# Optimization experiments

Hardware: AMD Instinct MI355X
Metric: run time of the kernel (lower is better)

## Reference

```python
import jax, jax.numpy as jnp
import numpy as np
import math

B, S, HID = 16, 512, 768
NUM_LABELS = 9
NUM_HEADS = 4
HEAD_DIM = HID // NUM_HEADS
MAX_REL = 5
B_PERSON = 1
I_PERSON = 2
LN_EPS = 1e-5


def setup_inputs() -> dict:
    key = jax.random.key(0)
    ks = jax.random.split(key, 16)
    w = lambda k, shp: jax.random.normal(k, shp, dtype=jnp.float32) * 0.02
    return {
        "sequence_output": jax.random.normal(ks[0], (B, S, HID), dtype=jnp.float32),
        "Wq": w(ks[1], (HID, HID)), "bq": jnp.zeros((HID,), jnp.float32),
        "Wk": w(ks[2], (HID, HID)), "bk": jnp.zeros((HID,), jnp.float32),
        "Wv": w(ks[3], (HID, HID)), "bv": jnp.zeros((HID,), jnp.float32),
        "Wo": w(ks[4], (HID, HID)), "bo": jnp.zeros((HID,), jnp.float32),
        "ln_g": jnp.ones((HID,), jnp.float32), "ln_b": jnp.zeros((HID,), jnp.float32),
        "Ws": w(ks[5], (HID, NUM_LABELS)), "bs": jnp.zeros((NUM_LABELS,), jnp.float32),
        "entity_bias": w(ks[6], (NUM_LABELS,)),
    }


def _heads(x):
    # [B,S,HID] -> [B,H,S,D]
    return x.reshape(B, S, NUM_HEADS, HEAD_DIM).transpose(0, 2, 1, 3)


def reference(sequence_output, Wq, bq, Wk, bk, Wv, bv, Wo, bo, ln_g, ln_b, Ws, bs, entity_bias):
    x = sequence_output
    q = _heads(x @ Wq + bq)
    k = _heads(x @ Wk + bk)
    v = _heads(x @ Wv + bv)

    scores = jnp.einsum("bhqd,bhkd->bhqk", q, k)
    # relative position bias: exp(-0.1 * clamp(|i-j|, 0, MAX_REL)), broadcast over b,h
    idx = jnp.arange(S, dtype=jnp.float32)
    dist = jnp.abs(idx[None, :] - idx[:, None])  # [S,S]
    rel_bias = jnp.exp(-0.1 * jnp.clip(dist, 0.0, float(MAX_REL)))
    dist_mask = -0.1 * dist
    scores = (scores + rel_bias) / math.sqrt(HEAD_DIM) + dist_mask
    probs = jax.nn.softmax(scores, axis=-1)  # dropout is identity in eval

    ctx = jnp.einsum("bhqk,bhkd->bhqd", probs, v)
    ctx = ctx.transpose(0, 2, 1, 3).reshape(B, S, HID)
    out = ctx @ Wo + bo

    h = x + out
    mu = jnp.mean(h, axis=-1, keepdims=True)
    var = jnp.mean(jnp.square(h - mu), axis=-1, keepdims=True)
    h = (h - mu) * jax.lax.rsqrt(var + LN_EPS) * ln_g + ln_b

    span_logits = h @ Ws + bs  # [B,S,L]
    # vectorized entity-bias post-process: the torch loop adds entity_bias[I_PERSON]
    # TWICE to final_logits[:, j, I_PERSON] whenever argmax(span_logits[:, j-1]) == B_PERSON
    prev_is_b = jnp.argmax(span_logits[:, :-1], axis=-1) == B_PERSON  # [B,S-1]
    bump = jnp.where(prev_is_b, 2.0 * entity_bias[I_PERSON], 0.0)
    final_logits = span_logits.at[:, 1:, I_PERSON].add(bump)
    return final_logits
```

## Files before the change

kernel.cpp:

```cpp
#include <hip/hip_runtime.h>
#include <math.h>

#define SEQ 512
#define HID 768
#define NBATCH 16
#define ROWS 8192
#define INV_SQRT_D 0.07216878364870323f

typedef short s8v __attribute__((ext_vector_type(8)));
typedef _Float16 h8v __attribute__((ext_vector_type(8)));
typedef float f4v __attribute__((ext_vector_type(4)));
typedef unsigned short u16;

__device__ __forceinline__ u16 f2h(float f) {
  _Float16 h = (_Float16)f;
  return __builtin_bit_cast(u16, h);
}

template <int KSTEPS>
__device__ __forceinline__ void mm_core128(
    const u16* __restrict__ A, const int lda,
    const u16* __restrict__ B, const int ldb,
    u16* lds, f4v (&acc)[4][4])
{
  const int tid = threadIdx.x;
  const int w = tid >> 6, ln = tid & 63;
  const u16* src = (w >> 1) ? B : A;
  const int ld = (w >> 1) ? ldb : lda;
  const int half = w & 1;
  const int srow = ln >> 2;
  const int csw  = ((ln & 3) - (ln >> 3)) & 3;
  const int ml = ln & 15, quad = ln >> 4;
  const int fo2 = ((quad + ((ln >> 1) & 3)) & 3) * 8;
  const int wr = (w >> 1) * 64, wc = (w & 1) * 64;

  const u16* gp[4];
  int lpo[4];
#pragma unroll
  for (int t = 0; t < 4; ++t) {
    const int row = half * 64 + t * 16 + srow;
    gp[t]  = src + (size_t)row * ld + csw * 8;
    lpo[t] = (w >> 1) * 4096 + half * 2048 + t * 512 + ln * 8;
  }
  s8v c[8];
#pragma unroll
  for (int t = 0; t < 4; ++t) {
    c[t]     = *(const s8v*)gp[t];
    c[4 + t] = *(const s8v*)(gp[t] + 32);
  }

  for (int kp = 0; kp < KSTEPS / 2; ++kp) {
    __syncthreads();
#pragma unroll
    for (int t = 0; t < 4; ++t) {
      *(s8v*)&lds[lpo[t]]        = c[t];
      *(s8v*)&lds[8192 + lpo[t]] = c[4 + t];
    }
    __syncthreads();
    if (kp + 1 < KSTEPS / 2) {
      const int k0 = (kp + 1) * 64;
#pragma unroll
      for (int t = 0; t < 4; ++t) {
        c[t]     = *(const s8v*)(gp[t] + k0);
        c[4 + t] = *(const s8v*)(gp[t] + k0 + 32);
      }
    }
#pragma unroll
    for (int sub = 0; sub < 2; ++sub) {
      const int so = sub * 8192;
      h8v a[4], b[4];
#pragma unroll
      for (int i = 0; i < 4; ++i)
        a[i] = *(const h8v*)&lds[so + (wr + i * 16 + ml) * 32 + fo2];
#pragma unroll
      for (int j = 0; j < 4; ++j)
        b[j] = *(const h8v*)&lds[so + 4096 + (wc + j * 16 + ml) * 32 + fo2];
#pragma unroll
      for (int i = 0; i < 4; ++i)
#pragma unroll
        for (int j = 0; j < 4; ++j)
          acc[i][j] = __builtin_amdgcn_mfma_f32_16x16x32_f16(a[i], b[j], acc[i][j], 0, 0, 0);
    }
  }
}

__global__ __launch_bounds__(256) void splitx(const float* __restrict__ x,
                                              u16* __restrict__ xh)
{
  const int i = blockIdx.x * 256 + threadIdx.x;
  const float4 v = ((const float4*)x)[i];
  ((ushort4*)xh)[i] = make_ushort4(f2h(v.x), f2h(v.y), f2h(v.z), f2h(v.w));
}

__global__ __launch_bounds__(256) void wsplit(
    const float* __restrict__ Wq, const float* __restrict__ Wk,
    const float* __restrict__ Wv, const float* __restrict__ Wo,
    u16* __restrict__ WTh)
{
  __shared__ float t[32][33];
  const int z = blockIdx.z;
  const float* W = (z == 0) ? Wq : (z == 1) ? Wk : (z == 2) ? Wv : Wo;
  const int n0 = blockIdx.x * 32, k0 = blockIdx.y * 32;
  const int tx = threadIdx.x & 31, ty = threadIdx.x >> 5;
#pragma unroll
  for (int i = 0; i < 4; ++i)
    t[ty + 8 * i][tx] = W[(size_t)(k0 + ty + 8 * i) * HID + n0 + tx];
  __syncthreads();
#pragma unroll
  for (int i = 0; i < 4; ++i) {
    const float v = t[tx][ty + 8 * i];
    const size_t idx = (size_t)z * HID * HID + (size_t)(n0 + ty + 8 * i) * HID + k0 + tx;
    WTh[idx] = f2h(v);
  }
}

__global__ __launch_bounds__(256, 3) void qkv_mm(
    const u16* __restrict__ xh, const u16* __restrict__ WTh,
    const float* __restrict__ bq, const float* __restrict__ bk, const float* __restrict__ bv,
    u16* __restrict__ qh, u16* __restrict__ kh, u16* __restrict__ vtmp16)
{
  __shared__ u16 lds[16384];
  const int id = blockIdx.x;
  const int xcd = id & 7;
  const int s = id >> 3;
  const int bx = s % 6;
  const int yl = (s / 6) & 7;
  const int z  = s / 48;
  const int bm = (yl * 8 + xcd) * 128;
  const int bn = bx * 128;
  const size_t wtoff = (size_t)z * HID * HID + (size_t)bn * HID;
  f4v acc[4][4];
#pragma unroll
  for (int i = 0; i < 4; ++i)
#pragma unroll
    for (int j = 0; j < 4; ++j) acc[i][j] = (f4v)0.f;
  mm_core128<24>(xh + (size_t)bm * HID, HID, WTh + wtoff, HID, lds, acc);
  const int tid = threadIdx.x, w = tid >> 6, ln = tid & 63;
  const int ml = ln & 15, quad = ln >> 4;
  const int wr = (w >> 1) * 64, wc = (w & 1) * 64;
  const float* bias = (z == 0) ? bq : (z == 1) ? bk : bv;
#pragma unroll
  for (int i = 0; i < 4; ++i)
#pragma unroll
    for (int j = 0; j < 4; ++j) {
      const int gcol = bn + wc + j * 16 + ml;
      const float bv_ = bias[gcol];
#pragma unroll
      for (int r = 0; r < 4; ++r) {
        const int grow = bm + wr + i * 16 + quad * 4 + r;
        const float v = acc[i][j][r] + bv_;
        const size_t idx = (size_t)grow * HID + gcol;
        if (z == 2)      vtmp16[idx] = f2h(v);
        else if (z == 0) qh[idx] = f2h(v);
        else             kh[idx] = f2h(v);
      }
    }
}

__global__ __launch_bounds__(256) void vtrans(const u16* __restrict__ vtmp16,
                                              u16* __restrict__ vTh)
{
  __shared__ u16 t[32][33];
  const int b = blockIdx.z, n0 = blockIdx.x * 32, c0 = blockIdx.y * 32;
  const int tx = threadIdx.x & 31, ty = threadIdx.x >> 5;
  const u16* src = vtmp16 + (size_t)b * SEQ * HID;
#pragma unroll
  for (int i = 0; i < 4; ++i)
    t[ty + 8 * i][tx] = src[(size_t)(c0 + ty + 8 * i) * HID + n0 + tx];
  __syncthreads();
#pragma unroll
  for (int i = 0; i < 4; ++i) {
    const size_t idx = (size_t)b * HID * SEQ + (size_t)(n0 + ty + 8 * i) * SEQ + c0 + tx;
    vTh[idx] = t[tx][ty + 8 * i];
  }
}

__global__ __launch_bounds__(256, 2) void scores_softmax(
    const u16* __restrict__ qh, const u16* __restrict__ kh, u16* __restrict__ P)
{
  __shared__ u16 lds[17408];
  __shared__ float red[4][32];
  const int z = blockIdx.y, b = z >> 2, hh = z & 3;
  const int bm = blockIdx.x * 32;
  const int tid = threadIdx.x, w = tid >> 6, ln = tid & 63;
  const int ml = ln & 15, quad = ln >> 4;
  const int fo2 = ((quad + ((ml >> 1) & 3)) & 3) * 8;
  const u16* qbase = qh + (size_t)(b * SEQ + bm) * HID + hh * 192;
  const u16* kbase = kh + (size_t)(b * SEQ) * HID + hh * 192;

  const int brow0 = tid >> 2, bsc = tid & 3;
  const u16* bgp[8];
  int blo[8];
#pragma unroll
  for (int t = 0; t < 8; ++t) {
    const int row = t * 64 + brow0;
    const int lc = (bsc - (row >> 1)) & 3;
    bgp[t] = kbase + (size_t)row * HID + lc * 8;
    blo[t] = 1024 + row * 32 + bsc * 8;
  }
  const bool hasA = tid < 128;
  const int arow = tid >> 2;
  const int alc = ((tid & 3) - (arow >> 1)) & 3;
  const u16* agp = qbase + (size_t)arow * HID + alc * 8;
  const int alo = arow * 32 + (tid & 3) * 8;

  s8v ca;
  s8v cb[8];
  if (hasA) ca = *(const s8v*)agp;
#pragma unroll
  for (int t = 0; t < 8; ++t) cb[t] = *(const s8v*)bgp[t];

  f4v acc[2][8];
#pragma unroll
  for (int i = 0; i < 2; ++i)
#pragma unroll
    for (int j = 0; j < 8; ++j) acc[i][j] = (f4v)0.f;

  for (int ks = 0; ks < 6; ++ks) {
    __syncthreads();
    if (hasA) *(s8v*)&lds[alo] = ca;
#pragma unroll
    for (int t = 0; t < 8; ++t) *(s8v*)&lds[blo[t]] = cb[t];
    __syncthreads();
    if (ks + 1 < 6) {
      const int k0 = (ks + 1) * 32;
      if (hasA) ca = *(const s8v*)(agp + k0);
#pragma unroll
      for (int t = 0; t < 8; ++t) cb[t] = *(const s8v*)(bgp[t] + k0);
    }
    h8v a[2];
#pragma unroll
    for (int i = 0; i < 2; ++i)
      a[i] = *(const h8v*)&lds[(i * 16 + ml) * 32 + fo2];
    h8v bfr[8];
#pragma unroll
    for (int j = 0; j < 8; ++j)
      bfr[j] = *(const h8v*)&lds[1024 + (w * 128 + j * 16 + ml) * 32 + fo2];
#pragma unroll
    for (int i = 0; i < 2; ++i)
#pragma unroll
      for (int j = 0; j < 8; ++j)
        acc[i][j] = __builtin_amdgcn_mfma_f32_16x16x32_f16(a[i], bfr[j], acc[i][j], 0, 0, 0);
  }

#pragma unroll
  for (int i = 0; i < 2; ++i)
#pragma unroll
    for (int j = 0; j < 8; ++j) {
      const int scol = w * 128 + j * 16 + ml;
#pragma unroll
      for (int r = 0; r < 4; ++r) {
        const int srow = bm + i * 16 + quad * 4 + r;
        const float dist = fabsf((float)(srow - scol));
        const float rel = __expf(-0.1f * fminf(dist, 5.0f));
        acc[i][j][r] = (acc[i][j][r] + rel) * INV_SQRT_D - 0.1f * dist;
      }
    }

  float mx[2][4];
#pragma unroll
  for (int i = 0; i < 2; ++i)
#pragma unroll
    for (int r = 0; r < 4; ++r) {
      float m = acc[i][0][r];
#pragma unroll
      for (int j = 1; j < 8; ++j) m = fmaxf(m, acc[i][j][r]);
#pragma unroll
      for (int o = 1; o < 16; o <<= 1) m = fmaxf(m, __shfl_xor(m, o, 64));
      mx[i][r] = m;
    }
  if (ml == 0) {
#pragma unroll
    for (int i = 0; i < 2; ++i)
#pragma unroll
      for (int r = 0; r < 4; ++r) red[w][i * 16 + quad * 4 + r] = mx[i][r];
  }
  __syncthreads();
#pragma unroll
  for (int i = 0; i < 2; ++i)
#pragma unroll
    for (int r = 0; r < 4; ++r) {
      const int R = i * 16 + quad * 4 + r;
      mx[i][r] = fmaxf(fmaxf(red[0][R], red[1][R]), fmaxf(red[2][R], red[3][R]));
    }
  __syncthreads();

  float sm[2][4];
#pragma unroll
  for (int i = 0; i < 2; ++i)
#pragma unroll
    for (int r = 0; r < 4; ++r) {
      float s = 0.f;
#pragma unroll
      for (int j = 0; j < 8; ++j) {
        const float p = __expf(acc[i][j][r] - mx[i][r]);
        acc[i][j][r] = p;
        s += p;
      }
#pragma unroll
      for (int o = 1; o < 16; o <<= 1) s += __shfl_xor(s, o, 64);
      sm[i][r] = s;
    }
  if (ml == 0) {
#pragma unroll
    for (int i = 0; i < 2; ++i)
#pragma unroll
      for (int r = 0; r < 4; ++r) red[w][i * 16 + quad * 4 + r] = sm[i][r];
  }
  __syncthreads();
#pragma unroll
  for (int i = 0; i < 2; ++i)
#pragma unroll
    for (int r = 0; r < 4; ++r) {
      const int R = i * 16 + quad * 4 + r;
      mx[i][r] = 1.0f / (red[0][R] + red[1][R] + red[2][R] + red[3][R]);
    }

  u16* Pz = P + (size_t)z * SEQ * SEQ;
#pragma unroll
  for (int i = 0; i < 2; ++i)
#pragma unroll
    for (int r = 0; r < 4; ++r) {
      const int row = bm + i * 16 + quad * 4 + r;
#pragma unroll
      for (int j = 0; j < 8; ++j) {
        const int scol = w * 128 + j * 16 + ml;
        Pz[(size_t)row * SEQ + scol] = f2h(acc[i][j][r] * mx[i][r]);
      }
    }
}

__global__ __launch_bounds__(256, 3) void pv_mm(
    const u16* __restrict__ P, const u16* __restrict__ vTh, u16* __restrict__ ch)
{
  __shared__ u16 lds[16384];
  const int z = blockIdx.y, b = z >> 2, hh = z & 3;
  const int bm = blockIdx.x * 64;
  const u16* ah_g = P + (size_t)z * SEQ * SEQ + (size_t)bm * SEQ;
  const u16* bh_g = vTh + (size_t)b * HID * SEQ + (size_t)(hh * 192) * SEQ;
  const int tid = threadIdx.x, w = tid >> 6, ln = tid & 63;
  const int srow = ln >> 2;
  const int csw  = ((ln & 3) - (ln >> 3)) & 3;
  const int schunk = csw * 8;
  const int ml = ln & 15, quad = ln >> 4;
  const int fo2 = ((quad + ((ln >> 1) & 3)) & 3) * 8;

  const u16* gp[4];
  int lpo[4];
#pragma unroll
  for (int s = 0; s < 4; ++s) {
    const int p = w * 4 + s;
    if (p < 4) {
      gp[s]  = ah_g + (size_t)(p * 16 + srow) * SEQ + schunk;
      lpo[s] = p * 512 + ln * 8;
    } else {
      const int t = p - 4;
      gp[s]  = bh_g + (size_t)(t * 16 + srow) * SEQ + schunk;
      lpo[s] = 2048 + t * 512 + ln * 8;
    }
  }
  s8v c[8];
#pragma unroll
  for (int s = 0; s < 4; ++s) {
    c[s]     = *(const s8v*)gp[s];
    c[4 + s] = *(const s8v*)(gp[s] + 32);
  }

  f4v acc[12];
#pragma unroll
  for (int j = 0; j < 12; ++j) acc[j] = (f4v)0.f;

  for (int kp = 0; kp < 8; ++kp) {
    __syncthreads();
#pragma unroll
    for (int s = 0; s < 4; ++s) {
      *(s8v*)&lds[lpo[s]]        = c[s];
      *(s8v*)&lds[8192 + lpo[s]] = c[4 + s];
    }
    __syncthreads();
    if (kp + 1 < 8) {
      const int k0 = (kp + 1) * 64;
#pragma unroll
      for (int s = 0; s < 4; ++s) {
        c[s]     = *(const s8v*)(gp[s] + k0);
        c[4 + s] = *(const s8v*)(gp[s] + k0 + 32);
      }
    }
#pragma unroll
    for (int sub = 0; sub < 2; ++sub) {
      const int so = sub * 8192;
      const h8v a = *(const h8v*)&lds[so + (w * 16 + ml) * 32 + fo2];
      h8v bfrag[12];
#pragma unroll
      for (int j = 0; j < 12; ++j)
        bfrag[j] = *(const h8v*)&lds[so + 2048 + (j * 16 + ml) * 32 + fo2];
#pragma unroll
      for (int j = 0; j < 12; ++j)
        acc[j] = __builtin_amdgcn_mfma_f32_16x16x32_f16(a, bfrag[j], acc[j], 0, 0, 0);
    }
  }
#pragma unroll
  for (int j = 0; j < 12; ++j) {
    const int gcol = hh * 192 + j * 16 + ml;
#pragma unroll
    for (int r = 0; r < 4; ++r) {
      const int m = bm + w * 16 + quad * 4 + r;
      const size_t idx = (size_t)(b * SEQ + m) * HID + gcol;
      ch[idx] = f2h(acc[j][r]);
    }
  }
}

__global__ __launch_bounds__(256, 3) void proj_mm(
    const u16* __restrict__ ch, const u16* __restrict__ WTh,
    const float* __restrict__ bo, const float* __restrict__ x, float* __restrict__ h)
{
  __shared__ u16 lds[16384];
  const int id = blockIdx.x;
  const int xcd = id & 7;
  const int s = id >> 3;
  const int bx = s % 6;
  const int yl = s / 6;
  const int bm = (yl * 8 + xcd) * 128;
  const int bn = bx * 128;
  const size_t wtoff = (size_t)3 * HID * HID + (size_t)bn * HID;
  f4v acc[4][4];
#pragma unroll
  for (int i = 0; i < 4; ++i)
#pragma unroll
    for (int j = 0; j < 4; ++j) acc[i][j] = (f4v)0.f;
  mm_core128<24>(ch + (size_t)bm * HID, HID, WTh + wtoff, HID, lds, acc);
  const int tid = threadIdx.x, w = tid >> 6, ln = tid & 63;
  const int ml = ln & 15, quad = ln >> 4;
  const int wr = (w >> 1) * 64, wc = (w & 1) * 64;
#pragma unroll
  for (int i = 0; i < 4; ++i)
#pragma unroll
    for (int j = 0; j < 4; ++j) {
      const int gcol = bn + wc + j * 16 + ml;
      const float bv_ = bo[gcol];
#pragma unroll
      for (int r = 0; r < 4; ++r) {
        const int grow = bm + wr + i * 16 + quad * 4 + r;
        const size_t idx = (size_t)grow * HID + gcol;
        h[idx] = acc[i][j][r] + bv_ + x[idx];
      }
    }
}

__global__ __launch_bounds__(256) void ln_logits_kernel(
    const float* __restrict__ h, const float* __restrict__ g,
    const float* __restrict__ bta, const float* __restrict__ Ws,
    const float* __restrict__ bsv, float* __restrict__ span)
{
  const int row = blockIdx.x;
  const int tid = threadIdx.x;
  const float* hr = h + (size_t)row * HID;
  const float x0 = hr[tid], x1 = hr[tid + 256], x2 = hr[tid + 512];
  float s = x0 + x1 + x2;
  float sq = x0 * x0 + x1 * x1 + x2 * x2;
#pragma unroll
  for (int o = 32; o > 0; o >>= 1) { s += __shfl_down(s, o, 64); sq += __shfl_down(sq, o, 64); }
  __shared__ float red[8];
  __shared__ float smu, srs;
  const int wid = tid >> 6, lid = tid & 63;
  if (lid == 0) { red[wid] = s; red[4 + wid] = sq; }
  __syncthreads();
  if (tid == 0) {
    const float ts = red[0] + red[1] + red[2] + red[3];
    const float tq = red[4] + red[5] + red[6] + red[7];
    const float mu = ts / 768.0f;
    const float var = tq / 768.0f - mu * mu;
    smu = mu; srs = rsqrtf(var + 1e-5f);
  }
  __syncthreads();
  const float mu = smu, rs = srs;
  const float n0 = (x0 - mu) * rs * g[tid] + bta[tid];
  const float n1 = (x1 - mu) * rs * g[tid + 256] + bta[tid + 256];
  const float n2 = (x2 - mu) * rs * g[tid + 512] + bta[tid + 512];
  float pl[9];
#pragma unroll
  for (int l = 0; l < 9; ++l)
    pl[l] = n0 * Ws[(size_t)tid * 9 + l]
          + n1 * Ws[(size_t)(tid + 256) * 9 + l]
          + n2 * Ws[(size_t)(tid + 512) * 9 + l];
#pragma unroll
  for (int l = 0; l < 9; ++l)
#pragma unroll
    for (int o = 32; o > 0; o >>= 1) pl[l] += __shfl_down(pl[l], o, 64);
  __shared__ float lred[4][9];
  if (lid == 0) {
#pragma unroll
    for (int l = 0; l < 9; ++l) lred[wid][l] = pl[l];
  }
  __syncthreads();
  if (tid < 9) {
    span[(size_t)row * 9 + tid] =
        lred[0][tid] + lred[1][tid] + lred[2][tid] + lred[3][tid] + bsv[tid];
  }
}

__global__ __launch_bounds__(256) void bump_kernel(
    const float* __restrict__ span, const float* __restrict__ eb, float* __restrict__ out)
{
  const int idx = blockIdx.x * 256 + threadIdx.x;
  if (idx >= ROWS) return;
  const int j = idx & (SEQ - 1);
  const float* sl = span + (size_t)idx * 9;
  float v[9];
#pragma unroll
  for (int l = 0; l < 9; ++l) v[l] = sl[l];
  if (j >= 1) {
    const float* sp = sl - 9;
    float m = sp[0]; int am = 0;
#pragma unroll
    for (int l = 1; l < 9; ++l) { const float t = sp[l]; if (t > m) { m = t; am = l; } }
    if (am == 1) v[2] += 2.0f * eb[2];
  }
#pragma unroll
  for (int l = 0; l < 9; ++l) out[(size_t)idx * 9 + l] = v[l];
}

extern "C" void kernel_launch(void* const* d_in, const int* in_sizes, int n_in,
                              void* d_out, int out_size, void* d_ws, size_t ws_size,
                              hipStream_t stream)
{
  (void)in_sizes; (void)n_in; (void)out_size; (void)ws_size;
  const float* x   = (const float*)d_in[0];
  const float* Wq  = (const float*)d_in[1];
  const float* bq  = (const float*)d_in[2];
  const float* Wk  = (const float*)d_in[3];
  const float* bk  = (const float*)d_in[4];
  const float* Wv  = (const float*)d_in[5];
  const float* bv  = (const float*)d_in[6];
  const float* Wo  = (const float*)d_in[7];
  const float* bo  = (const float*)d_in[8];
  const float* lng = (const float*)d_in[9];
  const float* lnb = (const float*)d_in[10];
  const float* Ws  = (const float*)d_in[11];
  const float* bs  = (const float*)d_in[12];
  const float* eb  = (const float*)d_in[13];
  float* out = (float*)d_out;

  char* ws = (char*)d_ws;
  u16* xh  = (u16*)(ws + 0);
  u16* vTh = xh;
  u16* WTh = (u16*)(ws + 25165824);
  u16* qh  = (u16*)(ws + 34603008);
  u16* kh  = (u16*)(ws + 59768832);
  u16* vtmp16 = (u16*)(ws + 84934656);
  float* hb = (float*)(ws + 84934656);
  u16* Pb  = (u16*)(ws + 117440512);
  float* spanb = (float*)(ws + 152043520);
  u16* ctxh = qh;

  splitx<<<dim3(1572864 / 256), 256, 0, stream>>>(x, xh);
  wsplit<<<dim3(24, 24, 4), 256, 0, stream>>>(Wq, Wk, Wv, Wo, WTh);
  qkv_mm<<<dim3(1152), 256, 0, stream>>>(xh, WTh, bq, bk, bv, qh, kh, vtmp16);
  vtrans<<<dim3(24, 16, 16), 256, 0, stream>>>(vtmp16, vTh);
  scores_softmax<<<dim3(16, 64), 256, 0, stream>>>(qh, kh, Pb);
  pv_mm<<<dim3(8, 64), 256, 0, stream>>>(Pb, vTh, ctxh);
  proj_mm<<<dim3(384), 256, 0, stream>>>(ctxh, WTh, bo, x, hb);
  ln_logits_kernel<<<dim3(ROWS), 256, 0, stream>>>(hb, lng, lnb, Ws, bs, spanb);
  bump_kernel<<<dim3(ROWS / 256), 256, 0, stream>>>(spanb, eb, out);
}
```

Measured before the change: 244.6 us.

## Fuse softmax probabilities with PV matmul, keeping P in LDS

Merges the scores/softmax kernel and the PV matmul kernel into one kernel. The normalized probability tile (32 rows x 512 keys) is written to swizzled LDS instead of global memory, then multiplied by streamed V^T tiles to produce context directly. This removes the global write and re-read of the full fp16 probability matrix and one kernel launch. In exchange, LDS use per block grows, and each 32-row block reloads all V for its head with less reuse than the old 64-row PV tiles.

```diff
diff --git a/kernel.cpp b/kernel.cpp
--- a/kernel.cpp
+++ b/kernel.cpp
@@ -175,10 +175,11 @@
   }
 }
 
-__global__ __launch_bounds__(256, 2) void scores_softmax(
-    const u16* __restrict__ qh, const u16* __restrict__ kh, u16* __restrict__ P)
-{
-  __shared__ u16 lds[17408];
+__global__ __launch_bounds__(256, 2) void attn_fused(
+    const u16* __restrict__ qh, const u16* __restrict__ kh,
+    const u16* __restrict__ vTh, u16* __restrict__ ch)
+{
+  __shared__ u16 lds[22528];
   __shared__ float red[4][32];
   const int z = blockIdx.y, b = z >> 2, hh = z & 3;
   const int bm = blockIdx.x * 32;
@@ -315,100 +316,80 @@
       const int R = i * 16 + quad * 4 + r;
       mx[i][r] = 1.0f / (red[0][R] + red[1][R] + red[2][R] + red[3][R]);
     }
-
-  u16* Pz = P + (size_t)z * SEQ * SEQ;
+  __syncthreads();
+
 #pragma unroll
   for (int i = 0; i < 2; ++i)
 #pragma unroll
     for (int r = 0; r < 4; ++r) {
-      const int row = bm + i * 16 + quad * 4 + r;
+      const int row = i * 16 + quad * 4 + r;
+      const int rsw = (row >> 1) & 3;
+      const int rbase = row * 512;
 #pragma unroll
       for (int j = 0; j < 8; ++j) {
-        const int scol = w * 128 + j * 16 + ml;
-        Pz[(size_t)row * SEQ + scol] = f2h(acc[i][j][r] * mx[i][r]);
-      }
-    }
-}
-
-__global__ __launch_bounds__(256, 3) void pv_mm(
-    const u16* __restrict__ P, const u16* __restrict__ vTh, u16* __restrict__ ch)
-{
-  __shared__ u16 lds[16384];
-  const int z = blockIdx.y, b = z >> 2, hh = z & 3;
-  const int bm = blockIdx.x * 64;
-  const u16* ah_g = P + (size_t)z * SEQ * SEQ + (size_t)bm * SEQ;
-  const u16* bh_g = vTh + (size_t)b * HID * SEQ + (size_t)(hh * 192) * SEQ;
-  const int tid = threadIdx.x, w = tid >> 6, ln = tid & 63;
-  const int srow = ln >> 2;
-  const int csw  = ((ln & 3) - (ln >> 3)) & 3;
-  const int schunk = csw * 8;
-  const int ml = ln & 15, quad = ln >> 4;
-  const int fo2 = ((quad + ((ln >> 1) & 3)) & 3) * 8;
-
-  const u16* gp[4];
-  int lpo[4];
-#pragma unroll
-  for (int s = 0; s < 4; ++s) {
-    const int p = w * 4 + s;
-    if (p < 4) {
-      gp[s]  = ah_g + (size_t)(p * 16 + srow) * SEQ + schunk;
-      lpo[s] = p * 512 + ln * 8;
-    } else {
-      const int t = p - 4;
-      gp[s]  = bh_g + (size_t)(t * 16 + srow) * SEQ + schunk;
-      lpo[s] = 2048 + t * 512 + ln * 8;
-    }
-  }
-  s8v c[8];
-#pragma unroll
-  for (int s = 0; s < 4; ++s) {
-    c[s]     = *(const s8v*)gp[s];
-    c[4 + s] = *(const s8v*)(gp[s] + 32);
-  }
-
-  f4v acc[12];
-#pragma unroll
-  for (int j = 0; j < 12; ++j) acc[j] = (f4v)0.f;
-
-  for (int kp = 0; kp < 8; ++kp) {
+        const int col = w * 128 + j * 16 + ml;
+        const int addr = rbase + (col & ~31) + ((((col >> 3) & 3) + rsw) & 3) * 8 + (col & 7);
+        lds[addr] = f2h(acc[i][j][r] * mx[i][r]);
+      }
+    }
+
+  const u16* vbase = vTh + (size_t)b * HID * SEQ + (size_t)(hh * 192) * SEQ;
+  const u16* vgp[3];
+  int vlo[3];
+#pragma unroll
+  for (int t = 0; t < 3; ++t) {
+    const int cch = t * 256 + tid;
+    const int vrow = cch >> 2, vsc = cch & 3;
+    const int vlc = (vsc - (vrow >> 1)) & 3;
+    vgp[t] = vbase + (size_t)vrow * SEQ + vlc * 8;
+    vlo[t] = 16384 + cch * 8;
+  }
+  s8v vc[3];
+#pragma unroll
+  for (int t = 0; t < 3; ++t) vc[t] = *(const s8v*)vgp[t];
+
+  f4v acc2[2][3];
+#pragma unroll
+  for (int i = 0; i < 2; ++i)
+#pragma unroll
+    for (int j = 0; j < 3; ++j) acc2[i][j] = (f4v)0.f;
+
+  for (int ks = 0; ks < 16; ++ks) {
     __syncthreads();
 #pragma unroll
-    for (int s = 0; s < 4; ++s) {
-      *(s8v*)&lds[lpo[s]]        = c[s];
-      *(s8v*)&lds[8192 + lpo[s]] = c[4 + s];
-    }
+    for (int t = 0; t < 3; ++t) *(s8v*)&lds[vlo[t]] = vc[t];
     __syncthreads();
-    if (kp + 1 < 8) {
-      const int k0 = (kp + 1) * 64;
-#pragma unroll
-      for (int s = 0; s < 4; ++s) {
-        c[s]     = *(const s8v*)(gp[s] + k0);
-        c[4 + s] = *(const s8v*)(gp[s] + k0 + 32);
-      }
-    }
-#pragma unroll
-    for (int sub = 0; sub < 2; ++sub) {
-      const int so = sub * 8192;
-      const h8v a = *(const h8v*)&lds[so + (w * 16 + ml) * 32 + fo2];
-      h8v bfrag[12];
-#pragma unroll
-      for (int j = 0; j < 12; ++j)
-        bfrag[j] = *(const h8v*)&lds[so + 2048 + (j * 16 + ml) * 32 + fo2];
-#pragma unroll
-      for (int j = 0; j < 12; ++j)
-        acc[j] = __builtin_amdgcn_mfma_f32_16x16x32_f16(a, bfrag[j], acc[j], 0, 0, 0);
-    }
-  }
-#pragma unroll
-  for (int j = 0; j < 12; ++j) {
-    const int gcol = hh * 192 + j * 16 + ml;
-#pragma unroll
-    for (int r = 0; r < 4; ++r) {
-      const int m = bm + w * 16 + quad * 4 + r;
-      const size_t idx = (size_t)(b * SEQ + m) * HID + gcol;
-      ch[idx] = f2h(acc[j][r]);
-    }
-  }
+    if (ks + 1 < 16) {
+      const int k0 = (ks + 1) * 32;
+#pragma unroll
+      for (int t = 0; t < 3; ++t) vc[t] = *(const s8v*)(vgp[t] + k0);
+    }
+    h8v a2[2];
+#pragma unroll
+    for (int i = 0; i < 2; ++i)
+      a2[i] = *(const h8v*)&lds[(i * 16 + ml) * 512 + ks * 32 + fo2];
+    h8v b2[3];
+#pragma unroll
+    for (int j = 0; j < 3; ++j)
+      b2[j] = *(const h8v*)&lds[16384 + (w * 48 + j * 16 + ml) * 32 + fo2];
+#pragma unroll
+    for (int i = 0; i < 2; ++i)
+#pragma unroll
+      for (int j = 0; j < 3; ++j)
+        acc2[i][j] = __builtin_amdgcn_mfma_f32_16x16x32_f16(a2[i], b2[j], acc2[i][j], 0, 0, 0);
+  }
+
+#pragma unroll
+  for (int i = 0; i < 2; ++i)
+#pragma unroll
+    for (int j = 0; j < 3; ++j) {
+      const int gcol = hh * 192 + w * 48 + j * 16 + ml;
+#pragma unroll
+      for (int r = 0; r < 4; ++r) {
+        const int m = bm + i * 16 + quad * 4 + r;
+        ch[(size_t)(b * SEQ + m) * HID + gcol] = f2h(acc2[i][j][r]);
+      }
+    }
 }
 
 __global__ __launch_bounds__(256, 3) void proj_mm(
@@ -550,7 +531,6 @@
   u16* kh  = (u16*)(ws + 59768832);
   u16* vtmp16 = (u16*)(ws + 84934656);
   float* hb = (float*)(ws + 84934656);
-  u16* Pb  = (u16*)(ws + 117440512);
   float* spanb = (float*)(ws + 152043520);
   u16* ctxh = qh;
 
@@ -558,8 +538,7 @@
   wsplit<<<dim3(24, 24, 4), 256, 0, stream>>>(Wq, Wk, Wv, Wo, WTh);
   qkv_mm<<<dim3(1152), 256, 0, stream>>>(xh, WTh, bq, bk, bv, qh, kh, vtmp16);
   vtrans<<<dim3(24, 16, 16), 256, 0, stream>>>(vtmp16, vTh);
-  scores_softmax<<<dim3(16, 64), 256, 0, stream>>>(qh, kh, Pb);
-  pv_mm<<<dim3(8, 64), 256, 0, stream>>>(Pb, vTh, ctxh);
+  attn_fused<<<dim3(16, 64), 256, 0, stream>>>(qh, kh, vTh, ctxh);
   proj_mm<<<dim3(384), 256, 0, stream>>>(ctxh, WTh, bo, x, hb);
   ln_logits_kernel<<<dim3(ROWS), 256, 0, stream>>>(hb, lng, lnb, Ws, bs, spanb);
   bump_kernel<<<dim3(ROWS / 256), 256, 0, stream>>>(spanb, eb, out);
```

Measured after the change: 234.4 us. -4.2%, faster.
